# Kernel tuning notes

Measured on AMD Instinct MI355X. Metric: run time of the kernel, lower is better.

The kernel has to match this reference:

```python
import jax, jax.numpy as jnp
import numpy as np

N, E, IN_DIM, HID, MAXW, HEADS = 20000, 640000, 128, 256, 512, 32
BN_EPS = 1e-5


def setup_inputs() -> dict:
    key = jax.random.key(0)
    ks = jax.random.split(key, 10)
    x = jax.random.normal(ks[0], (N, IN_DIM), dtype=jnp.float32)
    edge_index = jax.random.randint(ks[1], (2, E), 0, N, dtype=jnp.int64)
    s = 0.02
    # backbone GIN layer: Linear(in_dim -> hidden) applied to (x + sum of neighbors)
    Wb = jax.random.normal(ks[2], (IN_DIM, HID), dtype=jnp.float32) * s
    bb = jnp.zeros((HID,), dtype=jnp.float32)
    # per-head hourglass: Linear(HID->MAXW) + BN + ReLU, then Linear(MAXW->HID)
    W1 = jax.random.normal(ks[3], (HEADS, HID, MAXW), dtype=jnp.float32) * s
    b1 = jnp.zeros((HEADS, MAXW), dtype=jnp.float32)
    gamma = jnp.ones((HEADS, MAXW), dtype=jnp.float32)
    beta = jnp.zeros((HEADS, MAXW), dtype=jnp.float32)
    W2 = jax.random.normal(ks[4], (HEADS, MAXW, HID), dtype=jnp.float32) * s
    b2 = jnp.zeros((HEADS, HID), dtype=jnp.float32)
    return {"x": x, "edge_index": edge_index, "Wb": Wb, "bb": bb,
            "W1": W1, "b1": b1, "gamma": gamma, "beta": beta,
            "W2": W2, "b2": b2}


def reference(x, edge_index, Wb, bb, W1, b1, gamma, beta, W2, b2):
    src, dst = edge_index[0], edge_index[1]
    # GIN-style aggregation (eps=0): self + sum of neighbor features
    agg = x + jax.ops.segment_sum(x[src], dst, num_segments=x.shape[0])
    h = jax.nn.relu(agg @ Wb + bb)                          # [N, HID]
    # all 32 heads as one batched GEMM
    z = jnp.einsum('nd,hdm->hnm', h, W1) + b1[:, None, :]   # [H, N, MAXW]
    # per-head BatchNorm1d in training mode: batch stats over nodes, biased var
    mean = jnp.mean(z, axis=1, keepdims=True)
    var = jnp.var(z, axis=1, keepdims=True)
    zn = (z - mean) * jax.lax.rsqrt(var + BN_EPS)
    a = jax.nn.relu(zn * gamma[:, None, :] + beta[:, None, :])
    # final per-head projection, stacked to [N, H, HID]
    out = jnp.einsum('hnm,hmd->nhd', a, W2) + b2[None, :, :]
    return out
```

## Files before the change

### kernel.cpp

```cpp
#include <hip/hip_runtime.h>
#include <stdint.h>

#define N_NODES 20000
#define E_EDGES 640000
#define IN_DIM  128
#define HID     256
#define MAXW    512
#define HEADS   32
#define BN_EPS  1e-5f
#define NT      20480
#define NB_SCAN 79

typedef __attribute__((ext_vector_type(8))) short bf16x8;
typedef __attribute__((ext_vector_type(4))) float f32x4;
typedef __attribute__((ext_vector_type(16))) float f32x16;
typedef unsigned short ushort_t;

static __device__ __forceinline__ float bf2f(ushort_t u){
  union { unsigned int i; float f; } v; v.i = ((unsigned int)u) << 16; return v.f;
}
static __device__ __forceinline__ ushort_t f2bf(float f){
  union { float f; unsigned int i; } v; v.f = f;
  unsigned int r = v.i + 0x7fffu + ((v.i >> 16) & 1u);
  return (ushort_t)(r >> 16);
}

__global__ void k_initdet(const int* __restrict__ ei, float* __restrict__ G,
                          float* __restrict__ s, int* __restrict__ deg,
                          int* __restrict__ flag){
  int i = blockIdx.x * blockDim.x + threadIdx.x;
  int stride = gridDim.x * blockDim.x;
  float4 z4 = make_float4(0.f, 0.f, 0.f, 0.f);
  float4* Gd = (float4*)G;
  for (int j = i; j < 256 * 256 / 4; j += stride) Gd[j] = z4;
  for (int j = i; j < N_NODES; j += stride) deg[j] = 0;
  if (i < 256) s[i] = 0.f;
  if (blockIdx.x == 0){
    __shared__ int any_nz;
    if (threadIdx.x == 0) any_nz = 0;
    __syncthreads();
    int nz = 0;
    for (int k = threadIdx.x; k < 4096; k += blockDim.x)
      if (ei[2 * k + 1] != 0) nz = 1;
    if (nz) atomicOr(&any_nz, 1);
    __syncthreads();
    if (threadIdx.x == 0) flag[0] = (any_nz == 0) ? 1 : 0;
  }
}

__global__ __launch_bounds__(256) void k_hist(const int* __restrict__ ei,
                                              const int* __restrict__ flag,
                                              int* __restrict__ deg){
  int e = blockIdx.x * 256 + threadIdx.x;
  if (e >= E_EDGES) return;
  int src, dst;
  if (flag[0]){ src = ei[2 * e]; dst = ei[2 * E_EDGES + 2 * e]; }
  else        { src = ei[e];     dst = ei[E_EDGES + e]; }
  if ((unsigned)src >= N_NODES || (unsigned)dst >= N_NODES) return;
  atomicAdd(&deg[dst], 1);
}

__global__ __launch_bounds__(256) void k_scan1(const int* __restrict__ deg,
                                               int* __restrict__ bsum){
  __shared__ int ws[4];
  int b = blockIdx.x, t = threadIdx.x, i = b * 256 + t;
  int v = (i < N_NODES) ? deg[i] : 0;
  #pragma unroll
  for (int o = 32; o; o >>= 1) v += __shfl_down(v, o);
  if ((t & 63) == 0) ws[t >> 6] = v;
  __syncthreads();
  if (t == 0) bsum[b] = ws[0] + ws[1] + ws[2] + ws[3];
}

__global__ __launch_bounds__(64) void k_scan2(const int* __restrict__ bsum,
                                              int* __restrict__ boff){
  if (threadIdx.x == 0){
    int r = 0;
    for (int i = 0; i < NB_SCAN; i++){ boff[i] = r; r += bsum[i]; }
  }
}

__global__ __launch_bounds__(256) void k_scan3(const int* __restrict__ deg,
                                               const int* __restrict__ boff,
                                               int* __restrict__ start,
                                               int* __restrict__ cursor){
  __shared__ int a[2][256];
  int b = blockIdx.x, t = threadIdx.x, i = b * 256 + t;
  int v = (i < N_NODES) ? deg[i] : 0;
  a[0][t] = v;
  __syncthreads();
  int pb = 0;
  for (int o = 1; o < 256; o <<= 1){
    int x = a[pb][t] + ((t >= o) ? a[pb][t - o] : 0);
    a[pb ^ 1][t] = x;
    __syncthreads();
    pb ^= 1;
  }
  if (i < N_NODES){
    int ex = boff[b] + a[pb][t] - v;
    start[i] = ex; cursor[i] = ex;
  }
}

__global__ __launch_bounds__(256) void k_scatter(const int* __restrict__ ei,
                                                 const int* __restrict__ flag,
                                                 int* __restrict__ cursor,
                                                 int* __restrict__ eids){
  int e = blockIdx.x * 256 + threadIdx.x;
  if (e >= E_EDGES) return;
  int src, dst;
  if (flag[0]){ src = ei[2 * e]; dst = ei[2 * E_EDGES + 2 * e]; }
  else        { src = ei[e];     dst = ei[E_EDGES + e]; }
  if ((unsigned)src >= N_NODES || (unsigned)dst >= N_NODES) return;
  int p = atomicAdd(&cursor[dst], 1);
  eids[p] = src;
}

__global__ __launch_bounds__(256) void k_agg(const float* __restrict__ x,
                                             const int* __restrict__ start,
                                             const int* __restrict__ deg,
                                             const int* __restrict__ eids,
                                             float* __restrict__ agg){
  int wid = (blockIdx.x * 256 + threadIdx.x) >> 6;
  int lane = threadIdx.x & 63;
  if (wid >= N_NODES) return;
  int s0 = start[wid], d = deg[wid];
  float2 acc = *(const float2*)(x + (size_t)wid * IN_DIM + 2 * lane);
  int i = 0;
  for (; i + 4 <= d; i += 4){
    int e0 = eids[s0+i], e1 = eids[s0+i+1], e2 = eids[s0+i+2], e3 = eids[s0+i+3];
    float2 v0 = *(const float2*)(x + (size_t)e0 * IN_DIM + 2 * lane);
    float2 v1 = *(const float2*)(x + (size_t)e1 * IN_DIM + 2 * lane);
    float2 v2 = *(const float2*)(x + (size_t)e2 * IN_DIM + 2 * lane);
    float2 v3 = *(const float2*)(x + (size_t)e3 * IN_DIM + 2 * lane);
    acc.x += (v0.x + v1.x) + (v2.x + v3.x);
    acc.y += (v0.y + v1.y) + (v2.y + v3.y);
  }
  for (; i < d; i++){
    int e0 = eids[s0+i];
    float2 v0 = *(const float2*)(x + (size_t)e0 * IN_DIM + 2 * lane);
    acc.x += v0.x; acc.y += v0.y;
  }
  *(float2*)(agg + (size_t)wid * IN_DIM + 2 * lane) = acc;
}

__global__ __launch_bounds__(256) void k_backbone(const float* __restrict__ agg,
                                                  const float* __restrict__ Wb,
                                                  const float* __restrict__ bb,
                                                  ushort_t* __restrict__ hbf,
                                                  float* __restrict__ s){
  __shared__ float WbS[32][256];
  __shared__ float aggS[32][36];
  int c = threadIdx.x;
  int n0 = blockIdx.x * 32;
  float acc[32];
  float bias = bb[c];
  #pragma unroll
  for (int i = 0; i < 32; i++) acc[i] = bias;
  for (int dc = 0; dc < 4; ++dc){
    __syncthreads();
    const float4* wsrc = (const float4*)(Wb + dc * 32 * 256);
    float4* wdst = (float4*)&WbS[0][0];
    #pragma unroll
    for (int i = 0; i < 8; i++) wdst[c + i * 256] = wsrc[c + i * 256];
    {
      int n = c >> 3, c4 = (c & 7) * 4;
      float4 v = *(const float4*)(agg + (size_t)(n0 + n) * IN_DIM + dc * 32 + c4);
      aggS[n][c4 + 0] = v.x; aggS[n][c4 + 1] = v.y;
      aggS[n][c4 + 2] = v.z; aggS[n][c4 + 3] = v.w;
    }
    __syncthreads();
    for (int d = 0; d < 32; ++d){
      float w = WbS[d][c];
      #pragma unroll
      for (int n = 0; n < 32; n++) acc[n] += aggS[n][d] * w;
    }
  }
  float ls = 0.f;
  #pragma unroll
  for (int n = 0; n < 32; n++){
    float hv = acc[n] > 0.f ? acc[n] : 0.f;
    ushort_t hb = f2bf(hv);
    hbf[(size_t)(n0 + n) * HID + c] = hb;
    ls += bf2f(hb);
  }
  unsafeAtomicAdd(&s[c], ls);
}

__global__ __launch_bounds__(256) void k_htrans(const ushort_t* __restrict__ hbf,
                                                ushort_t* __restrict__ hT){
  __shared__ ushort_t tile[64][72];
  int n0 = blockIdx.x * 64;
  int c0 = blockIdx.y * 64;
  int t = threadIdx.x;
  int rowA = t >> 3, colO = t & 7;
  #pragma unroll
  for (int p = 0; p < 2; p++){
    int nl = rowA + p * 32;
    int n = n0 + nl;
    ushort_t tmp[8];
    if (n < N_NODES){
      *(uint4*)tmp = *(const uint4*)(hbf + (size_t)n * HID + c0 + colO * 8);
    } else {
      #pragma unroll
      for (int j = 0; j < 8; j++) tmp[j] = 0;
    }
    #pragma unroll
    for (int j = 0; j < 8; j++) tile[nl][colO * 8 + j] = tmp[j];
  }
  __syncthreads();
  #pragma unroll
  for (int p = 0; p < 2; p++){
    int cl = rowA + p * 32;
    ushort_t tmp[8];
    #pragma unroll
    for (int j = 0; j < 8; j++) tmp[j] = tile[colO * 8 + j][cl];
    *(uint4*)(hT + (size_t)(c0 + cl) * NT + n0 + colO * 8) = *(uint4*)tmp;
  }
}

__global__ __launch_bounds__(256) void k_gram2(const ushort_t* __restrict__ hT,
                                               float* __restrict__ G){
  const int t = threadIdx.x;
  const int w = t >> 6, l = t & 63;
  const int s = blockIdx.x, hh = blockIdx.y;
  const int wr = w >> 1, wc = w & 1;
  const int ca = hh * 128 + wr * 64;
  const int cb = wc * 128;
  const int l31 = l & 31, l5 = l >> 5;
  f32x16 acc[2][4];
  #pragma unroll
  for (int a = 0; a < 2; a++)
    #pragma unroll
    for (int b = 0; b < 4; b++)
      #pragma unroll
      for (int r = 0; r < 16; r++) acc[a][b][r] = 0.f;

  const size_t kb0 = (size_t)s * 512 + l5 * 8;
  for (int ks = 0; ks < 32; ks++){
    size_t k = kb0 + ks * 16;
    bf16x8 af[2], bfr[4];
    #pragma unroll
    for (int a = 0; a < 2; a++)
      af[a] = *(const bf16x8*)(hT + (size_t)(ca + a * 32 + l31) * NT + k);
    #pragma unroll
    for (int b = 0; b < 4; b++)
      bfr[b] = *(const bf16x8*)(hT + (size_t)(cb + b * 32 + l31) * NT + k);
    #pragma unroll
    for (int a = 0; a < 2; a++)
      #pragma unroll
      for (int b = 0; b < 4; b++)
        acc[a][b] = __builtin_amdgcn_mfma_f32_32x32x16_bf16(af[a], bfr[b], acc[a][b], 0, 0, 0);
  }
  #pragma unroll
  for (int a = 0; a < 2; a++)
    #pragma unroll
    for (int b = 0; b < 4; b++)
      #pragma unroll
      for (int r = 0; r < 16; r++){
        int grow = (r & 3) + 8 * (r >> 2) + 4 * l5;
        unsafeAtomicAdd(&G[(size_t)(ca + a * 32 + grow) * 256 + cb + b * 32 + l31], acc[a][b][r]);
      }
}

__global__ __launch_bounds__(256) void k_transpose(const float* __restrict__ W1,
                                                   const float* __restrict__ W2,
                                                   ushort_t* __restrict__ w1t,
                                                   ushort_t* __restrict__ w2t){
  __shared__ float tile[32][33];
  int which = blockIdx.z, h = blockIdx.y, b = blockIdx.x;
  const float* src; int R, C;
  if (which == 0){ src = W1 + (size_t)h * 256 * 512; R = 256; C = 512; }
  else           { src = W2 + (size_t)h * 512 * 256; R = 512; C = 256; }
  int tcn = C >> 5;
  int tr = b / tcn, tc = b % tcn;
  int r0 = tr * 32, c0 = tc * 32;
  int tx = threadIdx.x & 31, ty = threadIdx.x >> 5;
  #pragma unroll
  for (int i = 0; i < 32; i += 8) tile[ty + i][tx] = src[(size_t)(r0 + ty + i) * C + c0 + tx];
  __syncthreads();
  if (which == 0){
    ushort_t* dst = w1t + (size_t)h * 512 * 256;
    #pragma unroll
    for (int i = 0; i < 32; i += 8){
      int M = c0 + ty + i;
      int D = r0 + tx;
      int D2 = (((D >> 3) ^ (M & 7)) << 3) | (D & 7);
      dst[(size_t)M * 256 + D2] = f2bf(tile[tx][ty + i]);
    }
  } else {
    ushort_t* dst = w2t + (size_t)h * 256 * 512;
    #pragma unroll
    for (int i = 0; i < 32; i += 8){
      int dd = c0 + ty + i;
      int m  = r0 + tx;
      int g2 = ((m >> 3) & 3) ^ (dd & 3) ^ ((dd >> 2) & 3);
      size_t idx = (size_t)(m >> 5) * 8192 + dd * 32 + (g2 << 3) + (m & 7);
      dst[idx] = f2bf(tile[tx][ty + i]);
    }
  }
}

__global__ __launch_bounds__(256) void k_stats(const float* __restrict__ G,
                                               const float* __restrict__ s,
                                               const ushort_t* __restrict__ w1t,
                                               const float* __restrict__ b1,
                                               const float* __restrict__ gamma,
                                               const float* __restrict__ beta,
                                               float* __restrict__ As,
                                               float* __restrict__ Bs){
  __shared__ ushort_t wL[256][64];
  __shared__ float GL[16][256];
  __shared__ float sL[256];
  __shared__ float red[4][64];
  int h = blockIdx.y, m0 = blockIdx.x * 64;
  int t = threadIdx.x, m = t & 63, q = t >> 6;
  {
    int mm = t >> 2, part = t & 3;
    int Mrow = m0 + mm;
    const ushort_t* srcr = w1t + ((size_t)h * 512 + Mrow) * 256;
    #pragma unroll
    for (int k4 = 0; k4 < 16; ++k4){
      int kb = part * 64 + k4 * 4;
      int eo = (((kb >> 3) ^ (Mrow & 7)) << 3) | (kb & 7);
      ushort4 v = *(const ushort4*)(srcr + eo);
      wL[kb+0][mm]=v.x; wL[kb+1][mm]=v.y; wL[kb+2][mm]=v.z; wL[kb+3][mm]=v.w;
    }
  }
  sL[t & 255] = s[t & 255];
  float quad = 0.f;
  for (int dc = 0; dc < 16; ++dc){
    __syncthreads();
    const float4* gs = (const float4*)(G + (size_t)dc * 16 * 256);
    float4* gd = (float4*)&GL[0][0];
    #pragma unroll
    for (int i = 0; i < 4; i++) gd[t + i * 256] = gs[t + i * 256];
    __syncthreads();
    #pragma unroll
    for (int i = 0; i < 4; i++){
      int dl = q * 4 + i;
      float wd = bf2f(wL[dc * 16 + dl][m]);
      float u = 0.f;
      for (int k = 0; k < 256; ++k) u += GL[dl][k] * bf2f(wL[k][m]);
      quad += wd * u;
    }
  }
  red[q][m] = quad;
  __syncthreads();
  if (q == 0){
    float qd = red[0][m] + red[1][m] + red[2][m] + red[3][m];
    float dot_s = 0.f;
    for (int k = 0; k < 256; ++k) dot_s += sL[k] * bf2f(wL[k][m]);
    float b1v = b1[(size_t)h * 512 + m0 + m];
    float invN = 1.f / (float)N_NODES;
    float mean = dot_s * invN + b1v;
    float ez2 = (qd + 2.f * b1v * dot_s) * invN + b1v * b1v;
    float var = ez2 - mean * mean;
    float rstd = rsqrtf(var + BN_EPS);
    float gv = gamma[(size_t)h * 512 + m0 + m];
    float be = beta[(size_t)h * 512 + m0 + m];
    float Av = rstd * gv;
    As[(size_t)h * 512 + m0 + m] = Av;
    Bs[(size_t)h * 512 + m0 + m] = be - mean * Av;
  }
}

__global__ __launch_bounds__(512, 2) void k_main(const ushort_t* __restrict__ hbf,
                                                 const ushort_t* __restrict__ w1t,
                                                 const ushort_t* __restrict__ w2t,
                                                 const float* __restrict__ As,
                                                 const float* __restrict__ Bs,
                                                 const float* __restrict__ b2,
                                                 float* __restrict__ out){
  __shared__ __align__(16) char lds_all[65536];
  const int h = blockIdx.y;
  const int n0 = blockIdx.x * 256;
  const int t = threadIdx.x;
  const int w = t >> 6, l = t & 63;
  const int l15 = l & 15, l4 = l >> 4;
  const int nw = n0 + w * 32;
  const f32x4 fzero = {0.f, 0.f, 0.f, 0.f};
  const bf16x8 bzero = {0,0,0,0,0,0,0,0};

  bf16x8 afr[2][8];
  #pragma unroll
  for (int nset = 0; nset < 2; nset++){
    int row = nw + nset * 16 + l15;
    const ushort_t* p = hbf + (size_t)row * HID + l4 * 8;
    #pragma unroll
    for (int kk = 0; kk < 8; kk++){
      bf16x8 v = bzero;
      if (row < N_NODES) v = *(const bf16x8*)(p + kk * 32);
      afr[nset][kk] = v;
    }
  }
  f32x4 oacc[16][2];
  #pragma unroll
  for (int i = 0; i < 16; i++){ oacc[i][0] = fzero; oacc[i][1] = fzero; }

  const float* Asp = As + (size_t)h * 512;
  const float* Bsp = Bs + (size_t)h * 512;
  const char* w1g = (const char*)(w1t + (size_t)h * 512 * 256);
  const char* w2g = (const char*)(w2t + (size_t)h * 256 * 512);
  const int woff = w * 2048 + l * 16;

  {
    __builtin_amdgcn_global_load_lds((const __attribute__((address_space(1))) void*)(w1g + woff),
                                     (__attribute__((address_space(3))) void*)(lds_all + w * 2048), 16, 0, 0);
    __builtin_amdgcn_global_load_lds((const __attribute__((address_space(1))) void*)(w1g + woff + 1024),
                                     (__attribute__((address_space(3))) void*)(lds_all + w * 2048 + 1024), 16, 0, 0);
    __builtin_amdgcn_global_load_lds((const __attribute__((address_space(1))) void*)(w2g + woff),
                                     (__attribute__((address_space(3))) void*)(lds_all + 16384 + w * 2048), 16, 0, 0);
    __builtin_amdgcn_global_load_lds((const __attribute__((address_space(1))) void*)(w2g + woff + 1024),
                                     (__attribute__((address_space(3))) void*)(lds_all + 16384 + w * 2048 + 1024), 16, 0, 0);
  }
  __syncthreads();

  const int addrA = ((((l4 & 1) << 1) << 4) | l15) << 2;
  const int addrB = addrA + 64;
  const bool ct1 = (l4 >> 1) != 0;

  for (int c = 0; c < 16; ++c){
    const int cur = c & 1;
    const int mc0 = c * 32;
    const bool pf = (c < 15);
    if (pf){
      const int nb = (c + 1) * 16384;
      char* db = lds_all + (cur ^ 1) * 32768;
      __builtin_amdgcn_global_load_lds((const __attribute__((address_space(1))) void*)(w1g + nb + woff),
                                       (__attribute__((address_space(3))) void*)(db + w * 2048), 16, 0, 0);
      __builtin_amdgcn_global_load_lds((const __attribute__((address_space(1))) void*)(w1g + nb + woff + 1024),
                                       (__attribute__((address_space(3))) void*)(db + w * 2048 + 1024), 16, 0, 0);
      __builtin_amdgcn_global_load_lds((const __attribute__((address_space(1))) void*)(w2g + nb + woff),
                                       (__attribute__((address_space(3))) void*)(db + 16384 + w * 2048), 16, 0, 0);
      __builtin_amdgcn_global_load_lds((const __attribute__((address_space(1))) void*)(w2g + nb + woff + 1024),
                                       (__attribute__((address_space(3))) void*)(db + 16384 + w * 2048 + 1024), 16, 0, 0);
    }
    const char* w1b = lds_all + cur * 32768;
    const char* w2b = lds_all + cur * 32768 + 16384;

    f32x4 zt[2][2];
    zt[0][0] = fzero; zt[0][1] = fzero; zt[1][0] = fzero; zt[1][1] = fzero;
    __builtin_amdgcn_s_setprio(1);
    #pragma unroll
    for (int kk = 0; kk < 8; kk++){
      #pragma unroll
      for (int ct = 0; ct < 2; ct++){
        int r1 = ct * 16 + l15;
        int gr = kk * 4 + l4;
        bf16x8 wf = *(const bf16x8*)(w1b + r1 * 512 + ((gr ^ (r1 & 7)) * 16));
        zt[0][ct] = __builtin_amdgcn_mfma_f32_16x16x32_bf16(wf, afr[0][kk], zt[0][ct], 0, 0, 0);
        zt[1][ct] = __builtin_amdgcn_mfma_f32_16x16x32_bf16(wf, afr[1][kk], zt[1][ct], 0, 0, 0);
      }
    }
    __builtin_amdgcn_s_setprio(0);

    unsigned plo[2][2], phi[2][2];
    #pragma unroll
    for (int ct = 0; ct < 2; ct++){
      int mb = mc0 + ct * 16 + l4 * 4;
      float4 Av = *(const float4*)(Asp + mb);
      float4 Bv = *(const float4*)(Bsp + mb);
      #pragma unroll
      for (int nset = 0; nset < 2; nset++){
        float a0 = zt[nset][ct][0] * Av.x + Bv.x; a0 = a0 > 0.f ? a0 : 0.f;
        float a1 = zt[nset][ct][1] * Av.y + Bv.y; a1 = a1 > 0.f ? a1 : 0.f;
        float a2 = zt[nset][ct][2] * Av.z + Bv.z; a2 = a2 > 0.f ? a2 : 0.f;
        float a3 = zt[nset][ct][3] * Av.w + Bv.w; a3 = a3 > 0.f ? a3 : 0.f;
        plo[nset][ct] = (unsigned)f2bf(a0) | ((unsigned)f2bf(a1) << 16);
        phi[nset][ct] = (unsigned)f2bf(a2) | ((unsigned)f2bf(a3) << 16);
      }
    }
    bf16x8 aa[2];
    #pragma unroll
    for (int nset = 0; nset < 2; nset++){
      int q0a = __builtin_amdgcn_ds_bpermute(addrA, (int)plo[nset][0]);
      int q0b = __builtin_amdgcn_ds_bpermute(addrA, (int)plo[nset][1]);
      int q1a = __builtin_amdgcn_ds_bpermute(addrA, (int)phi[nset][0]);
      int q1b = __builtin_amdgcn_ds_bpermute(addrA, (int)phi[nset][1]);
      int q2a = __builtin_amdgcn_ds_bpermute(addrB, (int)plo[nset][0]);
      int q2b = __builtin_amdgcn_ds_bpermute(addrB, (int)plo[nset][1]);
      int q3a = __builtin_amdgcn_ds_bpermute(addrB, (int)phi[nset][0]);
      int q3b = __builtin_amdgcn_ds_bpermute(addrB, (int)phi[nset][1]);
      uint4 q;
      q.x = (unsigned)(ct1 ? q0b : q0a);
      q.y = (unsigned)(ct1 ? q1b : q1a);
      q.z = (unsigned)(ct1 ? q2b : q2a);
      q.w = (unsigned)(ct1 ? q3b : q3a);
      aa[nset] = *(bf16x8*)&q;
    }
    __builtin_amdgcn_s_setprio(1);
    #pragma unroll
    for (int ddt = 0; ddt < 16; ddt++){
      int dd = ddt * 16 + l15;
      int g2 = l4 ^ (dd & 3) ^ ((dd >> 2) & 3);
      bf16x8 wf2 = *(const bf16x8*)(w2b + dd * 64 + g2 * 16);
      oacc[ddt][0] = __builtin_amdgcn_mfma_f32_16x16x32_bf16(wf2, aa[0], oacc[ddt][0], 0, 0, 0);
      oacc[ddt][1] = __builtin_amdgcn_mfma_f32_16x16x32_bf16(wf2, aa[1], oacc[ddt][1], 0, 0, 0);
    }
    __builtin_amdgcn_s_setprio(0);

    __syncthreads();
  }

  char* slice = lds_all + w * 8192;
  const int gsl = l & 31;
  const int rhalf = l >> 5;
  #pragma unroll
  for (int nset = 0; nset < 2; nset++){
    #pragma unroll
    for (int half = 0; half < 2; half++){
      #pragma unroll
      for (int dq = 0; dq < 8; dq++){
        int ddt = half * 8 + dq;
        *(f32x4*)(slice + l15 * 512 + (((dq * 4 + l4) ^ (l15 & 7)) * 16)) = oacc[ddt][nset];
      }
      float4 b2v = *(const float4*)(b2 + (size_t)h * 256 + half * 128 + gsl * 4);
      #pragma unroll
      for (int j = 0; j < 8; j++){
        int rr = rhalf + j * 2;
        f32x4 v = *(const f32x4*)(slice + rr * 512 + ((gsl ^ (rr & 7)) * 16));
        int n = nw + nset * 16 + rr;
        if (n < N_NODES){
          float4 o;
          o.x = v[0] + b2v.x; o.y = v[1] + b2v.y;
          o.z = v[2] + b2v.z; o.w = v[3] + b2v.w;
          *(float4*)(out + (size_t)n * (HEADS * HID) + h * HID + half * 128 + gsl * 4) = o;
        }
      }
    }
  }
}

extern "C" void kernel_launch(void* const* d_in, const int* in_sizes, int n_in,
                              void* d_out, int out_size, void* d_ws, size_t ws_size,
                              hipStream_t stream){
  const float* x     = (const float*)d_in[0];
  const int*   ei    = (const int*)  d_in[1];
  const float* Wb    = (const float*)d_in[2];
  const float* bb    = (const float*)d_in[3];
  const float* W1    = (const float*)d_in[4];
  const float* b1    = (const float*)d_in[5];
  const float* gamma = (const float*)d_in[6];
  const float* beta  = (const float*)d_in[7];
  const float* W2    = (const float*)d_in[8];
  const float* b2    = (const float*)d_in[9];
  float* out = (float*)d_out;

  char* ws = (char*)d_ws;
  size_t off = 0;
  auto alloc = [&](size_t bytes){ void* p = ws + off; off += (bytes + 255) & ~(size_t)255; return p; };
  float*    agg  = (float*)   alloc((size_t)N_NODES * IN_DIM * 4);
  ushort_t* hbf  = (ushort_t*)alloc((size_t)N_NODES * HID * 2);
  ushort_t* w1t  = (ushort_t*)alloc((size_t)HEADS * MAXW * HID * 2);
  ushort_t* w2t  = (ushort_t*)alloc((size_t)HEADS * HID * MAXW * 2);
  float*    G    = (float*)   alloc(256 * 256 * 4);
  float*    s    = (float*)   alloc(256 * 4);
  float*    As   = (float*)   alloc((size_t)HEADS * MAXW * 4);
  float*    Bs   = (float*)   alloc((size_t)HEADS * MAXW * 4);
  int*      flg  = (int*)     alloc(256);
  int*      deg  = (int*)     alloc((size_t)N_NODES * 4);
  int*      st   = (int*)     alloc((size_t)N_NODES * 4);
  int*      cur  = (int*)     alloc((size_t)N_NODES * 4);
  int*      eids = (int*)     alloc((size_t)E_EDGES * 4);
  ushort_t* hT   = (ushort_t*)alloc((size_t)HID * NT * 2);
  int*      bsum = (int*)     alloc(NB_SCAN * 4);
  int*      boff = (int*)     alloc(NB_SCAN * 4);

  hipLaunchKernelGGL(k_initdet,   dim3(512),         dim3(256), 0, stream, ei, G, s, deg, flg);
  hipLaunchKernelGGL(k_hist,      dim3(2500),        dim3(256), 0, stream, ei, flg, deg);
  hipLaunchKernelGGL(k_scan1,     dim3(NB_SCAN),     dim3(256), 0, stream, deg, bsum);
  hipLaunchKernelGGL(k_scan2,     dim3(1),           dim3(64),  0, stream, bsum, boff);
  hipLaunchKernelGGL(k_scan3,     dim3(NB_SCAN),     dim3(256), 0, stream, deg, boff, st, cur);
  hipLaunchKernelGGL(k_scatter,   dim3(2500),        dim3(256), 0, stream, ei, flg, cur, eids);
  hipLaunchKernelGGL(k_agg,       dim3(5000),        dim3(256), 0, stream, x, st, deg, eids, agg);
  hipLaunchKernelGGL(k_backbone,  dim3(625),         dim3(256), 0, stream, agg, Wb, bb, hbf, s);
  hipLaunchKernelGGL(k_htrans,    dim3(320, 4),      dim3(256), 0, stream, hbf, hT);
  hipLaunchKernelGGL(k_gram2,     dim3(40, 2),       dim3(256), 0, stream, hT, G);
  hipLaunchKernelGGL(k_transpose, dim3(128, 32, 2),  dim3(256), 0, stream, W1, W2, w1t, w2t);
  hipLaunchKernelGGL(k_stats,     dim3(8, 32),       dim3(256), 0, stream, G, s, w1t, b1, gamma, beta, As, Bs);
  hipLaunchKernelGGL(k_main,      dim3(79, 32),      dim3(512), 0, stream, hbf, w1t, w2t, As, Bs, b2, out);
}
```

Measured before the change: 865.4 us.

## Fuse h transpose into backbone, fold scan2 into scan3, use LDS for activation relayout

The backbone kernel now writes the transposed bf16 h directly, and init zero-fills the padded tail of hT, which removes the separate transpose kernel. The single-thread block-offset scan kernel is dropped, and each scan3 block instead sums its preceding block totals itself. In the main kernel, the ds_bpermute shuffles that reshaped post-BN activations into MFMA A-fragments are replaced by a per-wave LDS staging area. That grows LDS to 80KB and adds a block-wide barrier per chunk, which may lower occupancy.

```diff
diff --git a/kernel.cpp b/kernel.cpp
--- a/kernel.cpp
+++ b/kernel.cpp
@@ -27,7 +27,7 @@
 
 __global__ void k_initdet(const int* __restrict__ ei, float* __restrict__ G,
                           float* __restrict__ s, int* __restrict__ deg,
-                          int* __restrict__ flag){
+                          int* __restrict__ flag, ushort_t* __restrict__ hT){
   int i = blockIdx.x * blockDim.x + threadIdx.x;
   int stride = gridDim.x * blockDim.x;
   float4 z4 = make_float4(0.f, 0.f, 0.f, 0.f);
@@ -35,6 +35,11 @@
   for (int j = i; j < 256 * 256 / 4; j += stride) Gd[j] = z4;
   for (int j = i; j < N_NODES; j += stride) deg[j] = 0;
   if (i < 256) s[i] = 0.f;
+  uint4 zi = make_uint4(0u, 0u, 0u, 0u);
+  for (int j = i; j < 256 * 60; j += stride){
+    int c = j / 60, o = (j % 60) * 8;
+    *(uint4*)(hT + (size_t)c * NT + N_NODES + o) = zi;
+  }
   if (blockIdx.x == 0){
     __shared__ int any_nz;
     if (threadIdx.x == 0) any_nz = 0;
@@ -72,20 +77,18 @@
   if (t == 0) bsum[b] = ws[0] + ws[1] + ws[2] + ws[3];
 }
 
-__global__ __launch_bounds__(64) void k_scan2(const int* __restrict__ bsum,
-                                              int* __restrict__ boff){
-  if (threadIdx.x == 0){
-    int r = 0;
-    for (int i = 0; i < NB_SCAN; i++){ boff[i] = r; r += bsum[i]; }
-  }
-}
-
 __global__ __launch_bounds__(256) void k_scan3(const int* __restrict__ deg,
-                                               const int* __restrict__ boff,
+                                               const int* __restrict__ bsum,
                                                int* __restrict__ start,
                                                int* __restrict__ cursor){
   __shared__ int a[2][256];
+  __shared__ int base;
   int b = blockIdx.x, t = threadIdx.x, i = b * 256 + t;
+  if (t == 0){
+    int r = 0;
+    for (int k = 0; k < b; k++) r += bsum[k];
+    base = r;
+  }
   int v = (i < N_NODES) ? deg[i] : 0;
   a[0][t] = v;
   __syncthreads();
@@ -97,7 +100,7 @@
     pb ^= 1;
   }
   if (i < N_NODES){
-    int ex = boff[b] + a[pb][t] - v;
+    int ex = base + a[pb][t] - v;
     start[i] = ex; cursor[i] = ex;
   }
 }
@@ -148,6 +151,7 @@
                                                   const float* __restrict__ Wb,
                                                   const float* __restrict__ bb,
                                                   ushort_t* __restrict__ hbf,
+                                                  ushort_t* __restrict__ hT,
                                                   float* __restrict__ s){
   __shared__ float WbS[32][256];
   __shared__ float aggS[32][36];
@@ -177,46 +181,19 @@
     }
   }
   float ls = 0.f;
+  ushort_t hrow[32];
   #pragma unroll
   for (int n = 0; n < 32; n++){
     float hv = acc[n] > 0.f ? acc[n] : 0.f;
     ushort_t hb = f2bf(hv);
     hbf[(size_t)(n0 + n) * HID + c] = hb;
+    hrow[n] = hb;
     ls += bf2f(hb);
   }
+  #pragma unroll
+  for (int i = 0; i < 4; i++)
+    *(uint4*)(hT + (size_t)c * NT + n0 + i * 8) = *(uint4*)(hrow + i * 8);
   unsafeAtomicAdd(&s[c], ls);
-}
-
-__global__ __launch_bounds__(256) void k_htrans(const ushort_t* __restrict__ hbf,
-                                                ushort_t* __restrict__ hT){
-  __shared__ ushort_t tile[64][72];
-  int n0 = blockIdx.x * 64;
-  int c0 = blockIdx.y * 64;
-  int t = threadIdx.x;
-  int rowA = t >> 3, colO = t & 7;
-  #pragma unroll
-  for (int p = 0; p < 2; p++){
-    int nl = rowA + p * 32;
-    int n = n0 + nl;
-    ushort_t tmp[8];
-    if (n < N_NODES){
-      *(uint4*)tmp = *(const uint4*)(hbf + (size_t)n * HID + c0 + colO * 8);
-    } else {
-      #pragma unroll
-      for (int j = 0; j < 8; j++) tmp[j] = 0;
-    }
-    #pragma unroll
-    for (int j = 0; j < 8; j++) tile[nl][colO * 8 + j] = tmp[j];
-  }
-  __syncthreads();
-  #pragma unroll
-  for (int p = 0; p < 2; p++){
-    int cl = rowA + p * 32;
-    ushort_t tmp[8];
-    #pragma unroll
-    for (int j = 0; j < 8; j++) tmp[j] = tile[colO * 8 + j][cl];
-    *(uint4*)(hT + (size_t)(c0 + cl) * NT + n0 + colO * 8) = *(uint4*)tmp;
-  }
 }
 
 __global__ __launch_bounds__(256) void k_gram2(const ushort_t* __restrict__ hT,
@@ -372,7 +349,7 @@
                                                  const float* __restrict__ Bs,
                                                  const float* __restrict__ b2,
                                                  float* __restrict__ out){
-  __shared__ __align__(16) char lds_all[65536];
+  __shared__ __align__(16) char lds_all[81920];
   const int h = blockIdx.y;
   const int n0 = blockIdx.x * 256;
   const int t = threadIdx.x;
@@ -381,6 +358,7 @@
   const int nw = n0 + w * 32;
   const f32x4 fzero = {0.f, 0.f, 0.f, 0.f};
   const bf16x8 bzero = {0,0,0,0,0,0,0,0};
+  char* asw = lds_all + 65536 + w * 2048;
 
   bf16x8 afr[2][8];
   #pragma unroll
@@ -415,10 +393,6 @@
                                      (__attribute__((address_space(3))) void*)(lds_all + 16384 + w * 2048 + 1024), 16, 0, 0);
   }
   __syncthreads();
-
-  const int addrA = ((((l4 & 1) << 1) << 4) | l15) << 2;
-  const int addrB = addrA + 64;
-  const bool ct1 = (l4 >> 1) != 0;
 
   for (int c = 0; c < 16; ++c){
     const int cur = c & 1;
@@ -455,7 +429,6 @@
     }
     __builtin_amdgcn_s_setprio(0);
 
-    unsigned plo[2][2], phi[2][2];
     #pragma unroll
     for (int ct = 0; ct < 2; ct++){
       int mb = mc0 + ct * 16 + l4 * 4;
@@ -467,28 +440,16 @@
         float a1 = zt[nset][ct][1] * Av.y + Bv.y; a1 = a1 > 0.f ? a1 : 0.f;
         float a2 = zt[nset][ct][2] * Av.z + Bv.z; a2 = a2 > 0.f ? a2 : 0.f;
         float a3 = zt[nset][ct][3] * Av.w + Bv.w; a3 = a3 > 0.f ? a3 : 0.f;
-        plo[nset][ct] = (unsigned)f2bf(a0) | ((unsigned)f2bf(a1) << 16);
-        phi[nset][ct] = (unsigned)f2bf(a2) | ((unsigned)f2bf(a3) << 16);
+        uint2 pk;
+        pk.x = (unsigned)f2bf(a0) | ((unsigned)f2bf(a1) << 16);
+        pk.y = (unsigned)f2bf(a2) | ((unsigned)f2bf(a3) << 16);
+        *(uint2*)(asw + (nset * 16 + l15) * 64 + ct * 32 + l4 * 8) = pk;
       }
     }
     bf16x8 aa[2];
-    #pragma unroll
-    for (int nset = 0; nset < 2; nset++){
-      int q0a = __builtin_amdgcn_ds_bpermute(addrA, (int)plo[nset][0]);
-      int q0b = __builtin_amdgcn_ds_bpermute(addrA, (int)plo[nset][1]);
-      int q1a = __builtin_amdgcn_ds_bpermute(addrA, (int)phi[nset][0]);
-      int q1b = __builtin_amdgcn_ds_bpermute(addrA, (int)phi[nset][1]);
-      int q2a = __builtin_amdgcn_ds_bpermute(addrB, (int)plo[nset][0]);
-      int q2b = __builtin_amdgcn_ds_bpermute(addrB, (int)plo[nset][1]);
-      int q3a = __builtin_amdgcn_ds_bpermute(addrB, (int)phi[nset][0]);
-      int q3b = __builtin_amdgcn_ds_bpermute(addrB, (int)phi[nset][1]);
-      uint4 q;
-      q.x = (unsigned)(ct1 ? q0b : q0a);
-      q.y = (unsigned)(ct1 ? q1b : q1a);
-      q.z = (unsigned)(ct1 ? q2b : q2a);
-      q.w = (unsigned)(ct1 ? q3b : q3a);
-      aa[nset] = *(bf16x8*)&q;
-    }
+    aa[0] = *(const bf16x8*)(asw + l15 * 64 + l4 * 16);
+    aa[1] = *(const bf16x8*)(asw + (16 + l15) * 64 + l4 * 16);
+
     __builtin_amdgcn_s_setprio(1);
     #pragma unroll
     for (int ddt = 0; ddt < 16; ddt++){
@@ -528,6 +489,7 @@
           *(float4*)(out + (size_t)n * (HEADS * HID) + h * HID + half * 128 + gsl * 4) = o;
         }
       }
+      __syncthreads();
     }
   }
 }
@@ -565,17 +527,14 @@
   int*      eids = (int*)     alloc((size_t)E_EDGES * 4);
   ushort_t* hT   = (ushort_t*)alloc((size_t)HID * NT * 2);
   int*      bsum = (int*)     alloc(NB_SCAN * 4);
-  int*      boff = (int*)     alloc(NB_SCAN * 4);
-
-  hipLaunchKernelGGL(k_initdet,   dim3(512),         dim3(256), 0, stream, ei, G, s, deg, flg);
+
+  hipLaunchKernelGGL(k_initdet,   dim3(512),         dim3(256), 0, stream, ei, G, s, deg, flg, hT);
   hipLaunchKernelGGL(k_hist,      dim3(2500),        dim3(256), 0, stream, ei, flg, deg);
   hipLaunchKernelGGL(k_scan1,     dim3(NB_SCAN),     dim3(256), 0, stream, deg, bsum);
-  hipLaunchKernelGGL(k_scan2,     dim3(1),           dim3(64),  0, stream, bsum, boff);
-  hipLaunchKernelGGL(k_scan3,     dim3(NB_SCAN),     dim3(256), 0, stream, deg, boff, st, cur);
+  hipLaunchKernelGGL(k_scan3,     dim3(NB_SCAN),     dim3(256), 0, stream, deg, bsum, st, cur);
   hipLaunchKernelGGL(k_scatter,   dim3(2500),        dim3(256), 0, stream, ei, flg, cur, eids);
   hipLaunchKernelGGL(k_agg,       dim3(5000),        dim3(256), 0, stream, x, st, deg, eids, agg);
-  hipLaunchKernelGGL(k_backbone,  dim3(625),         dim3(256), 0, stream, agg, Wb, bb, hbf, s);
-  hipLaunchKernelGGL(k_htrans,    dim3(320, 4),      dim3(256), 0, stream, hbf, hT);
+  hipLaunchKernelGGL(k_backbone,  dim3(625),         dim3(256), 0, stream, agg, Wb, bb, hbf, hT, s);
   hipLaunchKernelGGL(k_gram2,     dim3(40, 2),       dim3(256), 0, stream, hT, G);
   hipLaunchKernelGGL(k_transpose, dim3(128, 32, 2),  dim3(256), 0, stream, W1, W2, w1t, w2t);
   hipLaunchKernelGGL(k_stats,     dim3(8, 32),       dim3(256), 0, stream, G, s, w1t, b1, gamma, beta, As, Bs);
```

Result: no change. 878.9 us (+1.6%).
